# Performance work log

Hardware: AMD Instinct MI355X
Metric: run time of the kernel (lower is better)

Reference implementation:

```python
import jax, jax.numpy as jnp
import numpy as np

EMBED = 1024
HEADS = 16
HEAD_DIM = EMBED // HEADS


def setup_inputs() -> dict:
    key = jax.random.key(0)
    k1, k2, k3, k4, k5 = jax.random.split(key, 5)
    N, S = 2, 2048
    values = jax.random.normal(k1, (N, S, EMBED), dtype=jnp.float32)
    keys = jax.random.normal(k2, (N, S, EMBED), dtype=jnp.float32)
    query = jax.random.normal(k3, (N, S, EMBED), dtype=jnp.float32)
    mask = jnp.ones((N, 1, S, S), dtype=jnp.int32)
    # fc_out: Linear(heads*head_dim, embed_size) with bias; torch stores W as [out, in]
    W_out = jax.random.normal(k4, (EMBED, EMBED), dtype=jnp.float32) / np.sqrt(EMBED)
    b_out = jax.random.normal(k5, (EMBED,), dtype=jnp.float32) * 0.01
    return {"values": values, "keys": keys, "query": query, "mask": mask,
            "W_out": W_out, "b_out": b_out}


def reference(values, keys, query, mask, W_out, b_out):
    N, S, E = query.shape
    H, D = HEADS, HEAD_DIM
    # NOTE: source module never applies its q/k/v Linear layers (bug preserved).
    v = values.reshape(N, S, H, D)
    k = keys.reshape(N, S, H, D)
    q = query.reshape(N, S, H, D)
    energy = jnp.einsum('nqhd,nkhd->nhqk', q, k)  # [N,H,S,S]
    energy = jnp.where(mask == 0, jnp.float32(-1e20), energy)
    # non-standard scale: sqrt(embed_size), faithful to source
    attn = jax.nn.softmax(energy / jnp.sqrt(jnp.float32(E)), axis=3)
    out = jnp.einsum('nhql,nlhd->nqhd', attn, v).reshape(N, S, H * D)
    return out @ W_out.T + b_out
```

## Files before the change

kernel.cpp:

```cpp
#include <hip/hip_runtime.h>
#include <stdint.h>

#define S_LEN 2048
#define EMB 1024
#define NHEADS 16
#define HD 64
#define LOG2E 1.4426950408889634f

typedef __bf16 bf16x8 __attribute__((ext_vector_type(8)));
typedef float f32x4 __attribute__((ext_vector_type(4)));
typedef unsigned short u16;

#define MFMA16(a, b, c) __builtin_amdgcn_mfma_f32_16x16x32_bf16(a, b, c, 0, 0, 0)
#define GLOAD_LDS16(gp, lp)                                        \
  __builtin_amdgcn_global_load_lds(                                \
      (const __attribute__((address_space(1))) unsigned int*)(gp), \
      (__attribute__((address_space(3))) unsigned int*)(lp), 16, 0, 0)

__device__ __forceinline__ u16 bf16r(float x) {
  union { float f; unsigned int u; } c; c.f = x;
  unsigned int u = c.u + 0x7fffu + ((c.u >> 16) & 1u);
  return (u16)(u >> 16);
}

__device__ __forceinline__ unsigned int cvt_pk_bf16(float lo, float hi) {
  unsigned int r;
  asm("v_cvt_pk_bf16_f32 %0, %1, %2" : "=v"(r) : "v"(lo), "v"(hi));
  return r;
}

__device__ __forceinline__ float fexp2(float x) {
  float r;
  asm("v_exp_f32 %0, %1" : "=v"(r) : "v"(x));
  return r;
}

__global__ __launch_bounds__(256) void prep_kernel(
    const float* __restrict__ values, const float* __restrict__ keys,
    const float* __restrict__ W, const int* __restrict__ mask,
    u16* __restrict__ vt, u16* __restrict__ kb, u16* __restrict__ wb,
    unsigned char* __restrict__ fl2) {
  __shared__ u16 tile[64][65];
  __shared__ int s_ok[4];
  int b = blockIdx.x;
  int t = threadIdx.x;
  if (b < 1024) {
    int st = b & 31, h = (b >> 5) & 15, n = b >> 9;
    int s0 = st * 64;
    int d = t & 63, r4 = t >> 6;
#pragma unroll
    for (int i = 0; i < 16; ++i) {
      int s = r4 + i * 4;
      float x = values[(size_t)(n * S_LEN + s0 + s) * EMB + h * HD + d];
      tile[s][d] = bf16r(x);
    }
    __syncthreads();
#pragma unroll
    for (int i = 0; i < 16; ++i) {
      int dd = r4 + i * 4;
      vt[(size_t)((n * NHEADS + h) * HD + dd) * S_LEN + s0 + d] = tile[d][dd];
    }
  } else if (b < 2048) {
    int idx = (b - 1024) * 256 + t;
    const float4* in4 = (const float4*)keys;
    ushort4* out4 = (ushort4*)kb;
#pragma unroll
    for (int j = 0; j < 4; ++j) {
      float4 v = in4[idx + j * 262144];
      ushort4 o;
      o.x = bf16r(v.x); o.y = bf16r(v.y); o.z = bf16r(v.z); o.w = bf16r(v.w);
      out4[idx + j * 262144] = o;
    }
  } else if (b < 2304) {
    int idx = (b - 2048) * 256 + t;
    const float4* in4 = (const float4*)W;
    ushort4* out4 = (ushort4*)wb;
#pragma unroll
    for (int j = 0; j < 4; ++j) {
      float4 v = in4[idx + j * 65536];
      ushort4 o;
      o.x = bf16r(v.x); o.y = bf16r(v.y); o.z = bf16r(v.z); o.w = bf16r(v.w);
      out4[idx + j * 65536] = o;
    }
  } else {
    int idx = b - 2304;
    int kt = idx & 31, qt = (idx >> 5) & 15, n = idx >> 9;
    int qr = t >> 1, c8 = t & 1;
    const int4* mp = (const int4*)(mask + (size_t)n * S_LEN * S_LEN +
                                   (size_t)(qt * 128 + qr) * S_LEN + kt * 64) + c8 * 8;
    int ok = 1;
#pragma unroll
    for (int i = 0; i < 8; ++i) {
      int4 m = mp[i];
      ok &= (m.x != 0) & (m.y != 0) & (m.z != 0) & (m.w != 0);
    }
    ok = __all(ok);
    if ((t & 63) == 0) s_ok[t >> 6] = ok;
    __syncthreads();
    if (t == 0) fl2[idx] = (unsigned char)(s_ok[0] & s_ok[1] & s_ok[2] & s_ok[3]);
  }
}

__global__ __launch_bounds__(256) void attn_kernel(
    const float* __restrict__ query, const u16* __restrict__ kbuf,
    const u16* __restrict__ vt, const int* __restrict__ mask,
    const unsigned char* __restrict__ fl2, u16* __restrict__ ob) {
  __shared__ __align__(16) unsigned char kl[2][8192];
  __shared__ __align__(16) unsigned char vl[2][8192];
  __shared__ __align__(16) u16 pl[4][2][16][72];

  int b = blockIdx.x;
  b = (b & 7) * 64 + (b >> 3);
  int qt = b & 15, h = (b >> 4) & 15, n = b >> 8;
  int t = threadIdx.x, w = t >> 6, l = t & 63, l16 = l & 15, g = l >> 4;
  int q0w = qt * 128 + w * 32;

  bf16x8 aq[2][2];
#pragma unroll
  for (int u = 0; u < 2; ++u)
#pragma unroll
    for (int hh = 0; hh < 2; ++hh) {
      const float* qp = query + (size_t)(n * S_LEN + q0w + u * 16 + l16) * EMB +
                        h * HD + hh * 32 + g * 8;
      float4 f0 = *(const float4*)qp;
      float4 f1 = *(const float4*)(qp + 4);
      union { bf16x8 v; unsigned int u32[4]; } qq;
      qq.u32[0] = cvt_pk_bf16(f0.x * 0.03125f, f0.y * 0.03125f);
      qq.u32[1] = cvt_pk_bf16(f0.z * 0.03125f, f0.w * 0.03125f);
      qq.u32[2] = cvt_pk_bf16(f1.x * 0.03125f, f1.y * 0.03125f);
      qq.u32[3] = cvt_pk_bf16(f1.z * 0.03125f, f1.w * 0.03125f);
      aq[u][hh] = qq.v;
    }

  f32x4 zero4 = {0.f, 0.f, 0.f, 0.f};
  f32x4 acc[2][4];
  float lrun[2] = {0.f, 0.f}, mrun[2] = {0.f, 0.f}, mL[2] = {0.f, 0.f};
#pragma unroll
  for (int u = 0; u < 2; ++u)
#pragma unroll
    for (int db = 0; db < 4; ++db) acc[u][db] = zero4;

  int row_s = t >> 3, cc = t & 7;
  int sc = cc ^ (row_s & 7);
  const u16* gk0 = kbuf + (size_t)(n * S_LEN + row_s) * EMB + h * HD + sc * 8;
  const u16* gv0 = vt + (size_t)((n * NHEADS + h) * HD + row_s) * S_LEN + sc * 8;

  auto stage = [&](int kt, int nb) {
    const u16* gk = gk0 + (size_t)kt * 64 * EMB;
    const u16* gv = gv0 + kt * 64;
    GLOAD_LDS16(gk, kl[nb] + (w * 64) * 16);
    GLOAD_LDS16(gk + 32 * EMB, kl[nb] + (256 + w * 64) * 16);
    GLOAD_LDS16(gv, vl[nb] + (w * 64) * 16);
    GLOAD_LDS16(gv + 32 * S_LEN, vl[nb] + (256 + w * 64) * 16);
  };

  stage(0, 0);
  __syncthreads();

  for (int kt = 0; kt < S_LEN / 64; ++kt) {
    int cur = kt & 1;
    if (kt + 1 < S_LEN / 64) stage(kt + 1, cur ^ 1);
    const unsigned char* kc = kl[cur];
    const unsigned char* vc = vl[cur];

    f32x4 sf[2][4];
    __builtin_amdgcn_s_setprio(1);
#pragma unroll
    for (int kb = 0; kb < 4; ++kb) {
      int row = kb * 16 + l16;
      const unsigned char* kr = kc + row * 128;
      int sw = (row & 7) << 4;
      bf16x8 bk0 = *(const bf16x8*)(kr + ((g * 16) ^ sw));
      bf16x8 bk1 = *(const bf16x8*)(kr + ((64 + g * 16) ^ sw));
#pragma unroll
      for (int u = 0; u < 2; ++u) {
        f32x4 z = zero4;
        z = MFMA16(bk0, aq[u][0], z);
        z = MFMA16(bk1, aq[u][1], z);
        sf[u][kb] = z;
      }
    }
    __builtin_amdgcn_s_setprio(0);

    unsigned char fflag = fl2[((n * 16 + qt) * 32) + kt];
    if (!fflag) {
#pragma unroll
      for (int u = 0; u < 2; ++u) {
        const int* mrow = mask + (size_t)n * S_LEN * S_LEN +
                          (size_t)(q0w + u * 16 + l16) * S_LEN + kt * 64 + g * 4;
#pragma unroll
        for (int kb = 0; kb < 4; ++kb) {
          int4 mm = *(const int4*)(mrow + kb * 16);
          if (mm.x == 0) sf[u][kb][0] = -30.f;
          if (mm.y == 0) sf[u][kb][1] = -30.f;
          if (mm.z == 0) sf[u][kb][2] = -30.f;
          if (mm.w == 0) sf[u][kb][3] = -30.f;
        }
      }
    }

#pragma unroll
    for (int u = 0; u < 2; ++u) {
      float lmax = sf[u][0][0];
#pragma unroll
      for (int kb = 0; kb < 4; ++kb)
#pragma unroll
        for (int r = 0; r < 4; ++r) lmax = fmaxf(lmax, sf[u][kb][r]);
      if (!__all(lmax <= mrun[u] + 8.f)) {
        float rmax = fmaxf(lmax, __shfl_xor(lmax, 16));
        rmax = fmaxf(rmax, __shfl_xor(rmax, 32));
        float Mn = fmaxf(mrun[u], rmax);
        float corr = fexp2((mrun[u] - Mn) * LOG2E);
        mrun[u] = Mn;
        mL[u] = Mn * LOG2E;
        lrun[u] *= corr;
#pragma unroll
        for (int r = 0; r < 4; ++r) {
          float ca = __shfl(corr, (l & 48) + (g << 2) + r);
#pragma unroll
          for (int db = 0; db < 4; ++db) acc[u][db][r] *= ca;
        }
      }
      float p[4][4];
#pragma unroll
      for (int kb = 0; kb < 4; ++kb)
#pragma unroll
        for (int r = 0; r < 4; ++r)
          p[kb][r] = fexp2(fmaf(sf[u][kb][r], LOG2E, -mL[u]));
      float s01 = (p[0][0] + p[0][1]) + (p[0][2] + p[0][3]);
      float s23 = (p[1][0] + p[1][1]) + (p[1][2] + p[1][3]);
      float s45 = (p[2][0] + p[2][1]) + (p[2][2] + p[2][3]);
      float s67 = (p[3][0] + p[3][1]) + (p[3][2] + p[3][3]);
      lrun[u] += (s01 + s23) + (s45 + s67);
#pragma unroll
      for (int kb = 0; kb < 4; ++kb) {
        uint2 pw;
        pw.x = cvt_pk_bf16(p[kb][0], p[kb][1]);
        pw.y = cvt_pk_bf16(p[kb][2], p[kb][3]);
        *(uint2*)(&pl[w][u][l16][kb * 16 + g * 4]) = pw;
      }
    }
    __builtin_amdgcn_wave_barrier();

    __builtin_amdgcn_s_setprio(1);
#pragma unroll
    for (int hh = 0; hh < 2; ++hh) {
      bf16x8 ap0 = *(const bf16x8*)(&pl[w][0][l16][hh * 32 + g * 8]);
      bf16x8 ap1 = *(const bf16x8*)(&pl[w][1][l16][hh * 32 + g * 8]);
#pragma unroll
      for (int db = 0; db < 4; ++db) {
        int d = db * 16 + l16;
        bf16x8 bv = *(const bf16x8*)(vc + d * 128 + ((hh * 64 + g * 16) ^ ((d & 7) << 4)));
        acc[0][db] = MFMA16(ap0, bv, acc[0][db]);
        acc[1][db] = MFMA16(ap1, bv, acc[1][db]);
      }
    }
    __builtin_amdgcn_s_setprio(0);

    __syncthreads();
  }

#pragma unroll
  for (int u = 0; u < 2; ++u) {
    float s = lrun[u];
    s += __shfl_xor(s, 16);
    s += __shfl_xor(s, 32);
    float rinv[4];
#pragma unroll
    for (int r = 0; r < 4; ++r) {
      float sr = __shfl(s, (l & 48) + (g << 2) + r);
      rinv[r] = 1.f / sr;
    }
#pragma unroll
    for (int db = 0; db < 4; ++db)
#pragma unroll
      for (int r = 0; r < 4; ++r) {
        int qg = q0w + u * 16 + (g << 2) + r;
        ob[(size_t)(n * S_LEN + qg) * EMB + h * HD + db * 16 + l16] =
            bf16r(acc[u][db][r] * rinv[r]);
      }
  }
}

__global__ __launch_bounds__(256) void proj_kernel(
    const u16* __restrict__ A, const u16* __restrict__ Bt,
    const float* __restrict__ bias, float* __restrict__ C) {
  __shared__ __align__(16) unsigned char al[2][16384];
  __shared__ __align__(16) unsigned char bl[2][16384];
  int bm = blockIdx.x, bn = blockIdx.y;
  int t = threadIdx.x, w = t >> 6, l = t & 63;
  int l16 = l & 15, g = l >> 4;
  int wm = w >> 1, wn = w & 1;
  f32x4 zero4 = {0.f, 0.f, 0.f, 0.f};
  f32x4 acc[4][4];
#pragma unroll
  for (int m = 0; m < 4; ++m)
#pragma unroll
    for (int nn = 0; nn < 4; ++nn) acc[m][nn] = zero4;
  int row_s = t >> 3, cc = t & 7;
  int sc = cc ^ (row_s & 7);
  const u16* ga0 = A + (size_t)(bm * 128 + row_s) * EMB + sc * 8;
  const u16* gb0 = Bt + (size_t)(bn * 128 + row_s) * EMB + sc * 8;

  auto stage = [&](int ks, int nb) {
#pragma unroll
    for (int i = 0; i < 4; ++i) {
      GLOAD_LDS16(ga0 + (size_t)i * 32 * EMB + ks * 64, al[nb] + (i * 256 + w * 64) * 16);
      GLOAD_LDS16(gb0 + (size_t)i * 32 * EMB + ks * 64, bl[nb] + (i * 256 + w * 64) * 16);
    }
  };

  stage(0, 0);
  __syncthreads();

  for (int ks = 0; ks < 16; ++ks) {
    int cur = ks & 1;
    if (ks + 1 < 16) stage(ks + 1, cur ^ 1);
    __builtin_amdgcn_s_setprio(1);
#pragma unroll
    for (int hh = 0; hh < 2; ++hh) {
      bf16x8 af[4], bfr[4];
#pragma unroll
      for (int m = 0; m < 4; ++m) {
        int row = wm * 64 + m * 16 + l16;
        af[m] = *(const bf16x8*)(al[cur] + row * 128 + ((hh * 64 + g * 16) ^ ((row & 7) << 4)));
      }
#pragma unroll
      for (int nn = 0; nn < 4; ++nn) {
        int row = wn * 64 + nn * 16 + l16;
        bfr[nn] = *(const bf16x8*)(bl[cur] + row * 128 + ((hh * 64 + g * 16) ^ ((row & 7) << 4)));
      }
#pragma unroll
      for (int m = 0; m < 4; ++m)
#pragma unroll
        for (int nn = 0; nn < 4; ++nn) acc[m][nn] = MFMA16(af[m], bfr[nn], acc[m][nn]);
    }
    __builtin_amdgcn_s_setprio(0);
    __syncthreads();
  }
#pragma unroll
  for (int nn = 0; nn < 4; ++nn) {
    int j = bn * 128 + wn * 64 + nn * 16 + l16;
    float bj = bias[j];
#pragma unroll
    for (int m = 0; m < 4; ++m) {
      int i0 = bm * 128 + wm * 64 + m * 16 + g * 4;
#pragma unroll
      for (int r = 0; r < 4; ++r) C[(size_t)(i0 + r) * EMB + j] = acc[m][nn][r] + bj;
    }
  }
}

extern "C" void kernel_launch(void* const* d_in, const int* in_sizes, int n_in,
                              void* d_out, int out_size, void* d_ws, size_t ws_size,
                              hipStream_t stream) {
  const float* values = (const float*)d_in[0];
  const float* keys = (const float*)d_in[1];
  const float* query = (const float*)d_in[2];
  const int* mask = (const int*)d_in[3];
  const float* W = (const float*)d_in[4];
  const float* bias = (const float*)d_in[5];
  float* out = (float*)d_out;

  u16* kb = (u16*)d_ws;
  u16* vt = kb + 4194304;
  u16* ob = vt + 4194304;
  u16* wb = ob + 4194304;
  unsigned char* fl2 = (unsigned char*)(wb + 1048576);

  prep_kernel<<<3328, 256, 0, stream>>>(values, keys, W, mask, vt, kb, wb, fl2);
  attn_kernel<<<512, 256, 0, stream>>>(query, kb, vt, mask, fl2, ob);
  proj_kernel<<<dim3(32, 8), 256, 0, stream>>>(ob, wb, bias, out);
}
```

Baseline: 100.5 us.

## Keep softmax probabilities in registers via permuted V layout; retile projection GEMM

```diff
diff --git a/kernel.cpp b/kernel.cpp
--- a/kernel.cpp
+++ b/kernel.cpp
@@ -33,6 +33,11 @@
   float r;
   asm("v_exp_f32 %0, %1" : "=v"(r) : "v"(x));
   return r;
+}
+
+__device__ __forceinline__ int kperm(int k) {
+  int kb = (k >> 4) & 3, g = (k >> 2) & 3, r = k & 3;
+  return (kb >> 1) * 32 + g * 8 + (kb & 1) * 4 + r;
 }
 
 __global__ __launch_bounds__(256) void prep_kernel(
@@ -55,10 +60,11 @@
       tile[s][d] = bf16r(x);
     }
     __syncthreads();
+    int sp = s0 + kperm(d);
 #pragma unroll
     for (int i = 0; i < 16; ++i) {
       int dd = r4 + i * 4;
-      vt[(size_t)((n * NHEADS + h) * HD + dd) * S_LEN + s0 + d] = tile[d][dd];
+      vt[(size_t)((n * NHEADS + h) * HD + dd) * S_LEN + sp] = tile[d][dd];
     }
   } else if (b < 2048) {
     int idx = (b - 1024) * 256 + t;
@@ -101,40 +107,40 @@
   }
 }
 
-__global__ __launch_bounds__(256) void attn_kernel(
+__global__ __launch_bounds__(256, 2) void attn_kernel(
     const float* __restrict__ query, const u16* __restrict__ kbuf,
     const u16* __restrict__ vt, const int* __restrict__ mask,
     const unsigned char* __restrict__ fl2, u16* __restrict__ ob) {
   __shared__ __align__(16) unsigned char kl[2][8192];
   __shared__ __align__(16) unsigned char vl[2][8192];
-  __shared__ __align__(16) u16 pl[4][2][16][72];
 
   int b = blockIdx.x;
   b = (b & 7) * 64 + (b >> 3);
   int qt = b & 15, h = (b >> 4) & 15, n = b >> 8;
   int t = threadIdx.x, w = t >> 6, l = t & 63, l16 = l & 15, g = l >> 4;
-  int q0w = qt * 128 + w * 32;
-
+  int q0 = qt * 128 + w * 32;
+
+  const float QS = 0.03125f * LOG2E;
   bf16x8 aq[2][2];
 #pragma unroll
   for (int u = 0; u < 2; ++u)
 #pragma unroll
     for (int hh = 0; hh < 2; ++hh) {
-      const float* qp = query + (size_t)(n * S_LEN + q0w + u * 16 + l16) * EMB +
+      const float* qp = query + (size_t)(n * S_LEN + q0 + u * 16 + l16) * EMB +
                         h * HD + hh * 32 + g * 8;
       float4 f0 = *(const float4*)qp;
       float4 f1 = *(const float4*)(qp + 4);
       union { bf16x8 v; unsigned int u32[4]; } qq;
-      qq.u32[0] = cvt_pk_bf16(f0.x * 0.03125f, f0.y * 0.03125f);
-      qq.u32[1] = cvt_pk_bf16(f0.z * 0.03125f, f0.w * 0.03125f);
-      qq.u32[2] = cvt_pk_bf16(f1.x * 0.03125f, f1.y * 0.03125f);
-      qq.u32[3] = cvt_pk_bf16(f1.z * 0.03125f, f1.w * 0.03125f);
+      qq.u32[0] = cvt_pk_bf16(f0.x * QS, f0.y * QS);
+      qq.u32[1] = cvt_pk_bf16(f0.z * QS, f0.w * QS);
+      qq.u32[2] = cvt_pk_bf16(f1.x * QS, f1.y * QS);
+      qq.u32[3] = cvt_pk_bf16(f1.z * QS, f1.w * QS);
       aq[u][hh] = qq.v;
     }
 
   f32x4 zero4 = {0.f, 0.f, 0.f, 0.f};
   f32x4 acc[2][4];
-  float lrun[2] = {0.f, 0.f}, mrun[2] = {0.f, 0.f}, mL[2] = {0.f, 0.f};
+  float lrun[2] = {0.f, 0.f}, mrun[2] = {0.f, 0.f};
 #pragma unroll
   for (int u = 0; u < 2; ++u)
 #pragma unroll
@@ -187,18 +193,19 @@
 #pragma unroll
       for (int u = 0; u < 2; ++u) {
         const int* mrow = mask + (size_t)n * S_LEN * S_LEN +
-                          (size_t)(q0w + u * 16 + l16) * S_LEN + kt * 64 + g * 4;
+                          (size_t)(q0 + u * 16 + l16) * S_LEN + kt * 64 + g * 4;
 #pragma unroll
         for (int kb = 0; kb < 4; ++kb) {
           int4 mm = *(const int4*)(mrow + kb * 16);
-          if (mm.x == 0) sf[u][kb][0] = -30.f;
-          if (mm.y == 0) sf[u][kb][1] = -30.f;
-          if (mm.z == 0) sf[u][kb][2] = -30.f;
-          if (mm.w == 0) sf[u][kb][3] = -30.f;
+          if (mm.x == 0) sf[u][kb][0] = -100.f;
+          if (mm.y == 0) sf[u][kb][1] = -100.f;
+          if (mm.z == 0) sf[u][kb][2] = -100.f;
+          if (mm.w == 0) sf[u][kb][3] = -100.f;
         }
       }
     }
 
+    bf16x8 pa[2][2];
 #pragma unroll
     for (int u = 0; u < 2; ++u) {
       float lmax = sf[u][0][0];
@@ -210,9 +217,8 @@
         float rmax = fmaxf(lmax, __shfl_xor(lmax, 16));
         rmax = fmaxf(rmax, __shfl_xor(rmax, 32));
         float Mn = fmaxf(mrun[u], rmax);
-        float corr = fexp2((mrun[u] - Mn) * LOG2E);
+        float corr = fexp2(mrun[u] - Mn);
         mrun[u] = Mn;
-        mL[u] = Mn * LOG2E;
         lrun[u] *= corr;
 #pragma unroll
         for (int r = 0; r < 4; ++r) {
@@ -226,35 +232,33 @@
       for (int kb = 0; kb < 4; ++kb)
 #pragma unroll
         for (int r = 0; r < 4; ++r)
-          p[kb][r] = fexp2(fmaf(sf[u][kb][r], LOG2E, -mL[u]));
+          p[kb][r] = fexp2(sf[u][kb][r] - mrun[u]);
       float s01 = (p[0][0] + p[0][1]) + (p[0][2] + p[0][3]);
       float s23 = (p[1][0] + p[1][1]) + (p[1][2] + p[1][3]);
       float s45 = (p[2][0] + p[2][1]) + (p[2][2] + p[2][3]);
       float s67 = (p[3][0] + p[3][1]) + (p[3][2] + p[3][3]);
       lrun[u] += (s01 + s23) + (s45 + s67);
 #pragma unroll
-      for (int kb = 0; kb < 4; ++kb) {
-        uint2 pw;
-        pw.x = cvt_pk_bf16(p[kb][0], p[kb][1]);
-        pw.y = cvt_pk_bf16(p[kb][2], p[kb][3]);
-        *(uint2*)(&pl[w][u][l16][kb * 16 + g * 4]) = pw;
-      }
-    }
-    __builtin_amdgcn_wave_barrier();
+      for (int hh = 0; hh < 2; ++hh) {
+        union { bf16x8 v; unsigned int u32[4]; } pp;
+        pp.u32[0] = cvt_pk_bf16(p[2 * hh][0], p[2 * hh][1]);
+        pp.u32[1] = cvt_pk_bf16(p[2 * hh][2], p[2 * hh][3]);
+        pp.u32[2] = cvt_pk_bf16(p[2 * hh + 1][0], p[2 * hh + 1][1]);
+        pp.u32[3] = cvt_pk_bf16(p[2 * hh + 1][2], p[2 * hh + 1][3]);
+        pa[u][hh] = pp.v;
+      }
+    }
 
     __builtin_amdgcn_s_setprio(1);
 #pragma unroll
-    for (int hh = 0; hh < 2; ++hh) {
-      bf16x8 ap0 = *(const bf16x8*)(&pl[w][0][l16][hh * 32 + g * 8]);
-      bf16x8 ap1 = *(const bf16x8*)(&pl[w][1][l16][hh * 32 + g * 8]);
+    for (int hh = 0; hh < 2; ++hh)
 #pragma unroll
       for (int db = 0; db < 4; ++db) {
         int d = db * 16 + l16;
         bf16x8 bv = *(const bf16x8*)(vc + d * 128 + ((hh * 64 + g * 16) ^ ((d & 7) << 4)));
-        acc[0][db] = MFMA16(ap0, bv, acc[0][db]);
-        acc[1][db] = MFMA16(ap1, bv, acc[1][db]);
-      }
-    }
+        acc[0][db] = MFMA16(pa[0][hh], bv, acc[0][db]);
+        acc[1][db] = MFMA16(pa[1][hh], bv, acc[1][db]);
+      }
     __builtin_amdgcn_s_setprio(0);
 
     __syncthreads();
@@ -275,7 +279,7 @@
     for (int db = 0; db < 4; ++db)
 #pragma unroll
       for (int r = 0; r < 4; ++r) {
-        int qg = q0w + u * 16 + (g << 2) + r;
+        int qg = q0 + u * 16 + (g << 2) + r;
         ob[(size_t)(n * S_LEN + qg) * EMB + h * HD + db * 16 + l16] =
             bf16r(acc[u][db][r] * rinv[r]);
       }
@@ -286,28 +290,28 @@
     const u16* __restrict__ A, const u16* __restrict__ Bt,
     const float* __restrict__ bias, float* __restrict__ C) {
   __shared__ __align__(16) unsigned char al[2][16384];
-  __shared__ __align__(16) unsigned char bl[2][16384];
+  __shared__ __align__(16) unsigned char bl[2][8192];
   int bm = blockIdx.x, bn = blockIdx.y;
   int t = threadIdx.x, w = t >> 6, l = t & 63;
   int l16 = l & 15, g = l >> 4;
-  int wm = w >> 1, wn = w & 1;
   f32x4 zero4 = {0.f, 0.f, 0.f, 0.f};
-  f32x4 acc[4][4];
-#pragma unroll
-  for (int m = 0; m < 4; ++m)
-#pragma unroll
-    for (int nn = 0; nn < 4; ++nn) acc[m][nn] = zero4;
+  f32x4 acc[2][4];
+#pragma unroll
+  for (int mi = 0; mi < 2; ++mi)
+#pragma unroll
+    for (int nj = 0; nj < 4; ++nj) acc[mi][nj] = zero4;
   int row_s = t >> 3, cc = t & 7;
   int sc = cc ^ (row_s & 7);
   const u16* ga0 = A + (size_t)(bm * 128 + row_s) * EMB + sc * 8;
-  const u16* gb0 = Bt + (size_t)(bn * 128 + row_s) * EMB + sc * 8;
+  const u16* gb0 = Bt + (size_t)(bn * 64 + row_s) * EMB + sc * 8;
 
   auto stage = [&](int ks, int nb) {
 #pragma unroll
-    for (int i = 0; i < 4; ++i) {
+    for (int i = 0; i < 4; ++i)
       GLOAD_LDS16(ga0 + (size_t)i * 32 * EMB + ks * 64, al[nb] + (i * 256 + w * 64) * 16);
+#pragma unroll
+    for (int i = 0; i < 2; ++i)
       GLOAD_LDS16(gb0 + (size_t)i * 32 * EMB + ks * 64, bl[nb] + (i * 256 + w * 64) * 16);
-    }
   };
 
   stage(0, 0);
@@ -319,34 +323,34 @@
     __builtin_amdgcn_s_setprio(1);
 #pragma unroll
     for (int hh = 0; hh < 2; ++hh) {
-      bf16x8 af[4], bfr[4];
-#pragma unroll
-      for (int m = 0; m < 4; ++m) {
-        int row = wm * 64 + m * 16 + l16;
-        af[m] = *(const bf16x8*)(al[cur] + row * 128 + ((hh * 64 + g * 16) ^ ((row & 7) << 4)));
-      }
-#pragma unroll
-      for (int nn = 0; nn < 4; ++nn) {
-        int row = wn * 64 + nn * 16 + l16;
-        bfr[nn] = *(const bf16x8*)(bl[cur] + row * 128 + ((hh * 64 + g * 16) ^ ((row & 7) << 4)));
-      }
-#pragma unroll
-      for (int m = 0; m < 4; ++m)
-#pragma unroll
-        for (int nn = 0; nn < 4; ++nn) acc[m][nn] = MFMA16(af[m], bfr[nn], acc[m][nn]);
+      bf16x8 af[2], bfr[4];
+#pragma unroll
+      for (int mi = 0; mi < 2; ++mi) {
+        int row = w * 32 + mi * 16 + l16;
+        af[mi] = *(const bf16x8*)(al[cur] + row * 128 + ((hh * 64 + g * 16) ^ ((row & 7) << 4)));
+      }
+#pragma unroll
+      for (int nj = 0; nj < 4; ++nj) {
+        int row = nj * 16 + l16;
+        bfr[nj] = *(const bf16x8*)(bl[cur] + row * 128 + ((hh * 64 + g * 16) ^ ((row & 7) << 4)));
+      }
+#pragma unroll
+      for (int mi = 0; mi < 2; ++mi)
+#pragma unroll
+        for (int nj = 0; nj < 4; ++nj) acc[mi][nj] = MFMA16(af[mi], bfr[nj], acc[mi][nj]);
     }
     __builtin_amdgcn_s_setprio(0);
     __syncthreads();
   }
 #pragma unroll
-  for (int nn = 0; nn < 4; ++nn) {
-    int j = bn * 128 + wn * 64 + nn * 16 + l16;
+  for (int nj = 0; nj < 4; ++nj) {
+    int j = bn * 64 + nj * 16 + l16;
     float bj = bias[j];
 #pragma unroll
-    for (int m = 0; m < 4; ++m) {
-      int i0 = bm * 128 + wm * 64 + m * 16 + g * 4;
-#pragma unroll
-      for (int r = 0; r < 4; ++r) C[(size_t)(i0 + r) * EMB + j] = acc[m][nn][r] + bj;
+    for (int mi = 0; mi < 2; ++mi) {
+      int i0 = bm * 128 + w * 32 + mi * 16 + g * 4;
+#pragma unroll
+      for (int r = 0; r < 4; ++r) C[(size_t)(i0 + r) * EMB + j] = acc[mi][nj][r] + bj;
     }
   }
 }
@@ -370,5 +374,5 @@
 
   prep_kernel<<<3328, 256, 0, stream>>>(values, keys, W, mask, vt, kb, wb, fl2);
   attn_kernel<<<512, 256, 0, stream>>>(query, kb, vt, mask, fl2, ob);
-  proj_kernel<<<dim3(32, 8), 256, 0, stream>>>(ob, wb, bias, out);
-}
+  proj_kernel<<<dim3(32, 16), 256, 0, stream>>>(ob, wb, bias, out);
+}
```

Result: faster. 90.23 us (-10.2%).
